# Performance work log

Measured on AMD Instinct MI355X. Metric: run time of the kernel, lower is better.

## Reference

```python
import jax, jax.numpy as jnp
import numpy as np

EPS = 1e-8  # denominator-FFT floor, as in torch_get_RTF


def setup_inputs() -> dict:
    key = jax.random.key(0)
    kx, kB = jax.random.split(key)
    Bsz, L, C, N = 8, 4096, 1024, 64
    x = jax.random.normal(kx, (Bsz, L, C), dtype=jnp.float32)
    A = jnp.zeros((C, N), dtype=jnp.float32)          # get_RTF: A = zeros
    B = jax.random.normal(kB, (C, N), dtype=jnp.float32)  # get_RTF: B = randn
    h0 = jnp.zeros((1,), dtype=jnp.float32)           # torch.tensor([0.])
    return {"x": x, "A": A, "B": B, "h0": h0}


def _rtf_kernel(A, B, L):
    """Rational transfer function kernel via frequency-domain division.
    A, B: (C, N) -> K: (C, L)."""
    N = A.shape[1]
    num = jnp.pad(B, ((0, 0), (1, L - N - 1)))            # (C, L)
    den = jnp.pad(A, ((0, 0), (1, L - N - 1))).at[:, 0].set(1.0)
    num_fft = jnp.fft.rfft(num)
    den_fft = jnp.fft.rfft(den)
    den_fft = jnp.where(jnp.abs(den_fft) < EPS,
                        jnp.asarray(EPS, den_fft.dtype), den_fft)
    return jnp.fft.irfft(num_fft / den_fft, n=L)          # (C, L)


def reference(x, A, B, h0):
    Bsz, L, C = x.shape
    K = _rtf_kernel(A, B, L)                              # (C, L)
    # FFT convolution: pad both kernel and input to length 2L along time.
    k_pad = jnp.pad(K, ((0, 0), (0, L)))                  # (C, 2L)
    u_pad = jnp.pad(x, ((0, 0), (0, L), (0, 0)))          # (Bsz, 2L, C)
    K_fft = jnp.fft.rfft(k_pad)                           # (C, L+1)
    u_fft = jnp.fft.rfft(u_pad.transpose(0, 2, 1))        # (Bsz, C, L+1)
    conv = jnp.fft.irfft(K_fft[None] * u_fft, n=2 * L)    # (Bsz, C, 2L)
    h1 = conv.transpose(0, 2, 1)[:, :L, :]                # (Bsz, L, C)
    y1 = h1 + h0 * x                                      # skip with learned scalar
    return jax.nn.gelu(y1, approximate=False)             # nn.GELU default = erf
```

## Files before the change

### kernel.cpp

```cpp
#include <hip/hip_runtime.h>
#include <math.h>


typedef float  v2f   __attribute__((ext_vector_type(2)));
typedef unsigned int v2u __attribute__((ext_vector_type(2)));
typedef float  f32x4 __attribute__((ext_vector_type(4)));
typedef short  s16x8 __attribute__((ext_vector_type(8)));
typedef short  s16x4 __attribute__((ext_vector_type(4)));

#define CBLK   32
#define TTILE  256
#define NT     8
#define BLOCK  512
#define NTAPS  64
#define GSTR   20
#define XCH    404
#define XOSTR  260

__device__ __forceinline__ short bf16_rne(float f) {
    unsigned u = __builtin_bit_cast(unsigned, f);
    unsigned r = (u + 0x7fffu + ((u >> 16) & 1u)) >> 16;
    return (short)r;
}
__device__ __forceinline__ float bf16_tof(short s) {
    unsigned u = ((unsigned)(unsigned short)s) << 16;
    return __builtin_bit_cast(float, u);
}

__device__ __forceinline__ v2f gelu2(v2f y) {
    const v2f one = (v2f)(1.0f);
    v2f z = y * (v2f)(0.70710678118654752f);
    v2f a = __builtin_elementwise_abs(z);
    v2f q = __builtin_elementwise_fma((v2f)(0.3275911f), a, one);
    v2f d;
    d.x = __builtin_amdgcn_rcpf(q.x);
    d.y = __builtin_amdgcn_rcpf(q.y);
    v2f p = (v2f)(1.061405429f);
    p = __builtin_elementwise_fma(p, d, (v2f)(-1.453152027f));
    p = __builtin_elementwise_fma(p, d, (v2f)( 1.421413741f));
    p = __builtin_elementwise_fma(p, d, (v2f)(-0.284496736f));
    p = __builtin_elementwise_fma(p, d, (v2f)( 0.254829592f));
    p = p * d;
    v2f nz2 = -(z * z);
    v2f e;
    e.x = __expf(nz2.x);
    e.y = __expf(nz2.y);
    v2f erfa = __builtin_elementwise_fma(-p, e, one);
    v2u sz = __builtin_bit_cast(v2u, z);
    v2u se = __builtin_bit_cast(v2u, erfa);
    v2u rr = (se & (v2u)(0x7fffffffu)) | (sz & (v2u)(0x80000000u));
    v2f erfz = __builtin_bit_cast(v2f, rr);
    return (v2f)(0.5f) * y * (one + erfz);
}

__global__ __launch_bounds__(BLOCK, 2)
void ssm_fir_gelu(const float* __restrict__ x,
                  const float* __restrict__ Bmat,
                  const float* __restrict__ h0,
                  float* __restrict__ out)
{
    __shared__ float xsf[TTILE * CBLK];
    __shared__ short xb[CBLK * XCH];
    __shared__ short xout[CBLK * XOSTR];

    const int tid   = threadIdx.x;
    const int wv    = tid >> 6, ln = tid & 63;
    const int half  = blockIdx.x;
    const int cbase = blockIdx.y * CBLK;
    const int b     = blockIdx.z;
    const int tbase = half * 2048;

    const int i_row = ln & 15;
    const int g     = ln >> 4;
    const int gh    = g >> 1, gl = g & 1;

    s16x8 afrag[4][4];
    #pragma unroll
    for (int c4 = 0; c4 < 4; ++c4) {
        const float* bp = Bmat + (size_t)(cbase + 4 * wv + c4) * NTAPS;
        #pragma unroll
        for (int jb = 0; jb < 4; ++jb) {
            #pragma unroll
            for (int e = 0; e < 8; ++e) {
                const int k  = 8 * g + e;
                const int jj = i_row - k + 15;
                float v = (jj >= 0 && jj < 16) ? bp[16 * jb + jj] : 0.f;
                afrag[c4][jb][e] = bf16_rne(v);
            }
        }
    }

    const float* gb = x + ((size_t)b * 4096) * 1024 + cbase + (ln & 7) * 4;
    const float h0v = h0[0];

    #define STAGE(T0)                                                         \
        {                                                                     \
            _Pragma("unroll")                                                 \
            for (int i = 0; i < 4; ++i) {                                     \
                const int c   = wv * 4 + i;                                   \
                const int row = 8 * c + (ln >> 3);                            \
                const int u   = (T0) + row;                                   \
                __builtin_amdgcn_global_load_lds(                             \
                    (const __attribute__((address_space(1))) void*)(gb + (size_t)u * 1024), \
                    (__attribute__((address_space(3))) void*)&xsf[c * 256],   \
                    16, 0, 0);                                                \
            }                                                                 \
        }

    #define CONVERT()                                                         \
        {                                                                     \
            _Pragma("unroll")                                                 \
            for (int p = 0; p < 4; ++p) {                                     \
                const int m   = tid + p * BLOCK;                              \
                const int chc = m & 31, rg = m >> 5;            \
                s16x4 pk;                                                     \
                _Pragma("unroll")                                             \
                for (int rr = 0; rr < 4; ++rr)                                \
                    pk[rr] = bf16_rne(xsf[(4 * rg + rr) * CBLK + chc]);       \
                *reinterpret_cast<s16x4*>(                                    \
                    &xb[chc * XCH + (4 + (rg >> 2)) * GSTR + 4 * (rg & 3)]) = pk; \
            }                                                                 \
        }

    #define COPYHALO()                                                        \
        {                                                                     \
            const int chc = tid & 31, sg = tid >> 5;            \
            const int so  = 4 * (sg & 3);                                     \
            s16x4 v = *reinterpret_cast<const s16x4*>(                        \
                &xb[chc * XCH + (16 + (sg >> 2)) * GSTR + so]);               \
            *reinterpret_cast<s16x4*>(                                        \
                &xb[chc * XCH + (sg >> 2) * GSTR + so]) = v;                  \
        }

    #define STORE(T0)                                                         \
        {                                                                     \
            _Pragma("unroll")                                                 \
            for (int p = 0; p < 4; ++p) {                                     \
                const int m = tid + p * BLOCK;                                \
                const int t = m >> 3, a = m & 7;                              \
                float4 o;                                                     \
                o.x = bf16_tof(xout[(4 * a + 0) * XOSTR + t]);                \
                o.y = bf16_tof(xout[(4 * a + 1) * XOSTR + t]);                \
                o.z = bf16_tof(xout[(4 * a + 2) * XOSTR + t]);                \
                o.w = bf16_tof(xout[(4 * a + 3) * XOSTR + t]);                \
                *reinterpret_cast<float4*>(                                   \
                    out + ((size_t)b * 4096 + (T0) + t) * 1024 + cbase + 4 * a) = o; \
            }                                                                 \
        }

    if (half == 0) {
        #pragma unroll
        for (int p = 0; p < 2; ++p) {
            const int m = tid + p * BLOCK;
            if (m < 640) {
                const int c = m & 31, wi = m >> 5;
                *reinterpret_cast<s16x4*>(&xb[c * XCH + 4 * wi]) = (s16x4)(short)0;
            }
        }
    } else {
        const int c   = wv;
        const int row = 8 * c + (ln >> 3);
        const int u   = tbase - 64 + row;
        __builtin_amdgcn_global_load_lds(
            (const __attribute__((address_space(1))) void*)(gb + (size_t)u * 1024),
            (__attribute__((address_space(3))) void*)&xsf[c * 256],
            16, 0, 0);
    }
    __syncthreads();
    if (half == 1) {
        const int chc = tid & 31, rg = tid >> 5;
        s16x4 pk;
        #pragma unroll
        for (int rr = 0; rr < 4; ++rr)
            pk[rr] = bf16_rne(xsf[(4 * rg + rr) * CBLK + chc]);
        *reinterpret_cast<s16x4*>(
            &xb[chc * XCH + (rg >> 2) * GSTR + 4 * (rg & 3)]) = pk;
    }
    __syncthreads();

    STAGE(tbase);
    __syncthreads();
    CONVERT();
    __syncthreads();
    STAGE(tbase + TTILE);

    #pragma unroll 1
    for (int k = 0; k < NT; ++k) {
        const int t0 = tbase + k * TTILE;

        #pragma unroll
        for (int c4 = 0; c4 < 4; ++c4) {
            const int chl = 4 * wv + c4;
            const short* xc = &xb[chl * XCH];

            f32x4 acc = (f32x4)(0.f);
            #pragma unroll
            for (int jb = 0; jb < 4; ++jb) {
                const int base = (3 - jb + i_row + gh) * GSTR + 8 * gl;
                const s16x4 lo = *reinterpret_cast<const s16x4*>(&xc[base]);
                const s16x4 hi = *reinterpret_cast<const s16x4*>(&xc[base + 4]);
                const s16x8 bfrag = __builtin_shufflevector(
                    lo, hi, 0, 1, 2, 3, 4, 5, 6, 7);
                acc = __builtin_amdgcn_mfma_f32_16x16x32_bf16(
                          afrag[c4][jb], bfrag, acc, 0, 0, 0);
            }

            const s16x4 xv4 = *reinterpret_cast<const s16x4*>(
                &xc[(4 + i_row) * GSTR + 4 * g]);
            v2f y01, y23;
            y01.x = acc[0] + h0v * bf16_tof(xv4[0]);
            y01.y = acc[1] + h0v * bf16_tof(xv4[1]);
            y23.x = acc[2] + h0v * bf16_tof(xv4[2]);
            y23.y = acc[3] + h0v * bf16_tof(xv4[3]);
            const v2f g01 = gelu2(y01), g23 = gelu2(y23);

            s16x4 opk;
            opk[0] = bf16_rne(g01.x);
            opk[1] = bf16_rne(g01.y);
            opk[2] = bf16_rne(g23.x);
            opk[3] = bf16_rne(g23.y);
            *reinterpret_cast<s16x4*>(
                &xout[chl * XOSTR + 16 * i_row + 4 * g]) = opk;
        }

        asm volatile("s_waitcnt vmcnt(0) lgkmcnt(0)" ::: "memory");
        __builtin_amdgcn_s_barrier();

        if (k < NT - 1) {
            COPYHALO();
            asm volatile("s_waitcnt lgkmcnt(0)" ::: "memory");
            __builtin_amdgcn_s_barrier();
            STORE(t0);
            CONVERT();
            asm volatile("s_waitcnt lgkmcnt(0)" ::: "memory");
            __builtin_amdgcn_s_barrier();
            if (k + 2 < NT) STAGE(tbase + (k + 2) * TTILE);
        } else {
            STORE(t0);
        }
    }
    #undef STAGE
    #undef CONVERT
    #undef COPYHALO
    #undef STORE
}

extern "C" void kernel_launch(void* const* d_in, const int* in_sizes, int n_in,
                              void* d_out, int out_size, void* d_ws, size_t ws_size,
                              hipStream_t stream) {
    const float* x    = (const float*)d_in[0];
    const float* Bmat = (const float*)d_in[2];
    const float* h0   = (const float*)d_in[3];
    float* out        = (float*)d_out;

    dim3 grid(2, 32, 8);
    ssm_fir_gelu<<<grid, dim3(BLOCK), 0, stream>>>(x, Bmat, h0, out);
}
```

Before: 62.41 us.

## Use circular LDS halo buffer to drop halo copy and barrier; widen stores

```diff
diff --git a/kernel.cpp b/kernel.cpp
--- a/kernel.cpp
+++ b/kernel.cpp
@@ -7,6 +7,7 @@
 typedef float  f32x4 __attribute__((ext_vector_type(4)));
 typedef short  s16x8 __attribute__((ext_vector_type(8)));
 typedef short  s16x4 __attribute__((ext_vector_type(4)));
+typedef short  s16x2 __attribute__((ext_vector_type(2)));
 
 #define CBLK   32
 #define TTILE  256
@@ -14,8 +15,9 @@
 #define BLOCK  512
 #define NTAPS  64
 #define GSTR   20
+#define NGRP   20
 #define XCH    404
-#define XOSTR  260
+#define XOSTR  262
 
 __device__ __forceinline__ short bf16_rne(float f) {
     unsigned u = __builtin_bit_cast(unsigned, f);
@@ -107,7 +109,7 @@
             }                                                                 \
         }
 
-    #define CONVERT()                                                         \
+    #define CONVERT(QBN)                                                      \
         {                                                                     \
             _Pragma("unroll")                                                 \
             for (int p = 0; p < 4; ++p) {                                     \
@@ -117,34 +119,33 @@
                 _Pragma("unroll")                                             \
                 for (int rr = 0; rr < 4; ++rr)                                \
                     pk[rr] = bf16_rne(xsf[(4 * rg + rr) * CBLK + chc]);       \
+                const int qr = (QBN) + 4 + (rg >> 2);                         \
+                const int qp = (qr >= NGRP) ? qr - NGRP : qr;                 \
                 *reinterpret_cast<s16x4*>(                                    \
-                    &xb[chc * XCH + (4 + (rg >> 2)) * GSTR + 4 * (rg & 3)]) = pk; \
+                    &xb[chc * XCH + qp * GSTR + 4 * (rg & 3)]) = pk;          \
             }                                                                 \
-        }
-
-    #define COPYHALO()                                                        \
-        {                                                                     \
-            const int chc = tid & 31, sg = tid >> 5;            \
-            const int so  = 4 * (sg & 3);                                     \
-            s16x4 v = *reinterpret_cast<const s16x4*>(                        \
-                &xb[chc * XCH + (16 + (sg >> 2)) * GSTR + so]);               \
-            *reinterpret_cast<s16x4*>(                                        \
-                &xb[chc * XCH + (sg >> 2) * GSTR + so]) = v;                  \
         }
 
     #define STORE(T0)                                                         \
         {                                                                     \
             _Pragma("unroll")                                                 \
-            for (int p = 0; p < 4; ++p) {                                     \
-                const int m = tid + p * BLOCK;                                \
-                const int t = m >> 3, a = m & 7;                              \
-                float4 o;                                                     \
-                o.x = bf16_tof(xout[(4 * a + 0) * XOSTR + t]);                \
-                o.y = bf16_tof(xout[(4 * a + 1) * XOSTR + t]);                \
-                o.z = bf16_tof(xout[(4 * a + 2) * XOSTR + t]);                \
-                o.w = bf16_tof(xout[(4 * a + 3) * XOSTR + t]);                \
-                *reinterpret_cast<float4*>(                                   \
-                    out + ((size_t)b * 4096 + (T0) + t) * 1024 + cbase + 4 * a) = o; \
+            for (int p = 0; p < 2; ++p) {                                     \
+                const int m  = tid + p * BLOCK;                               \
+                const int tp = m >> 3, a = m & 7;              \
+                const int t  = 2 * tp;                                        \
+                s16x2 r0 = *reinterpret_cast<const s16x2*>(&xout[(4*a+0)*XOSTR + t]); \
+                s16x2 r1 = *reinterpret_cast<const s16x2*>(&xout[(4*a+1)*XOSTR + t]); \
+                s16x2 r2 = *reinterpret_cast<const s16x2*>(&xout[(4*a+2)*XOSTR + t]); \
+                s16x2 r3 = *reinterpret_cast<const s16x2*>(&xout[(4*a+3)*XOSTR + t]); \
+                float4 o0, o1;                                                \
+                o0.x = bf16_tof(r0[0]); o0.y = bf16_tof(r1[0]);               \
+                o0.z = bf16_tof(r2[0]); o0.w = bf16_tof(r3[0]);               \
+                o1.x = bf16_tof(r0[1]); o1.y = bf16_tof(r1[1]);               \
+                o1.z = bf16_tof(r2[1]); o1.w = bf16_tof(r3[1]);               \
+                float* op = out + ((size_t)b * 4096 + (T0) + t) * 1024        \
+                                + cbase + 4 * a;                              \
+                *reinterpret_cast<float4*>(op)        = o0;                   \
+                *reinterpret_cast<float4*>(op + 1024) = o1;                   \
             }                                                                 \
         }
 
@@ -180,14 +181,18 @@
 
     STAGE(tbase);
     __syncthreads();
-    CONVERT();
+    CONVERT(0);
     __syncthreads();
     STAGE(tbase + TTILE);
+
+    int qb = 0;
 
     #pragma unroll 1
     for (int k = 0; k < NT; ++k) {
         const int t0 = tbase + k * TTILE;
 
+        const int q2r = qb + 4 + i_row;
+        const int q2  = (q2r >= NGRP) ? q2r - NGRP : q2r;
         #pragma unroll
         for (int c4 = 0; c4 < 4; ++c4) {
             const int chl = 4 * wv + c4;
@@ -196,7 +201,9 @@
             f32x4 acc = (f32x4)(0.f);
             #pragma unroll
             for (int jb = 0; jb < 4; ++jb) {
-                const int base = (3 - jb + i_row + gh) * GSTR + 8 * gl;
+                const int qr = qb + 3 - jb + i_row + gh;
+                const int qp = (qr >= NGRP) ? qr - NGRP : qr;
+                const int base = qp * GSTR + 8 * gl;
                 const s16x4 lo = *reinterpret_cast<const s16x4*>(&xc[base]);
                 const s16x4 hi = *reinterpret_cast<const s16x4*>(&xc[base + 4]);
                 const s16x8 bfrag = __builtin_shufflevector(
@@ -206,7 +213,7 @@
             }
 
             const s16x4 xv4 = *reinterpret_cast<const s16x4*>(
-                &xc[(4 + i_row) * GSTR + 4 * g]);
+                &xc[q2 * GSTR + 4 * g]);
             v2f y01, y23;
             y01.x = acc[0] + h0v * bf16_tof(xv4[0]);
             y01.y = acc[1] + h0v * bf16_tof(xv4[1]);
@@ -214,24 +221,22 @@
             y23.y = acc[3] + h0v * bf16_tof(xv4[3]);
             const v2f g01 = gelu2(y01), g23 = gelu2(y23);
 
-            s16x4 opk;
-            opk[0] = bf16_rne(g01.x);
-            opk[1] = bf16_rne(g01.y);
-            opk[2] = bf16_rne(g23.x);
-            opk[3] = bf16_rne(g23.y);
-            *reinterpret_cast<s16x4*>(
-                &xout[chl * XOSTR + 16 * i_row + 4 * g]) = opk;
+            s16x2 w0, w1;
+            w0[0] = bf16_rne(g01.x); w0[1] = bf16_rne(g01.y);
+            w1[0] = bf16_rne(g23.x); w1[1] = bf16_rne(g23.y);
+            short* xo = &xout[chl * XOSTR + 16 * i_row + 4 * g];
+            *reinterpret_cast<s16x2*>(xo)     = w0;
+            *reinterpret_cast<s16x2*>(xo + 2) = w1;
         }
 
         asm volatile("s_waitcnt vmcnt(0) lgkmcnt(0)" ::: "memory");
         __builtin_amdgcn_s_barrier();
 
         if (k < NT - 1) {
-            COPYHALO();
-            asm volatile("s_waitcnt lgkmcnt(0)" ::: "memory");
-            __builtin_amdgcn_s_barrier();
+            const int qbn = (qb + 16 >= NGRP) ? qb - 4 : qb + 16;
             STORE(t0);
-            CONVERT();
+            CONVERT(qbn);
+            qb = qbn;
             asm volatile("s_waitcnt lgkmcnt(0)" ::: "memory");
             __builtin_amdgcn_s_barrier();
             if (k + 2 < NT) STAGE(tbase + (k + 2) * TTILE);
@@ -241,7 +246,6 @@
     }
     #undef STAGE
     #undef CONVERT
-    #undef COPYHALO
     #undef STORE
 }
 
```

Result: slower. 64.85 us (+3.9%).
